# Kernel tuning notes

Measured on AMD Instinct MI355X. Metric: run time of the kernel, lower is better.

The kernel has to match this reference:

```python
import jax, jax.numpy as jnp
import numpy as np

N_NODES, N_EDGES = 1024, 4096
D_NODE, D_EDGE, HEADS, N_CLASSES = 128, 256, 4, 16


def setup_inputs() -> dict:
    key = jax.random.key(0)
    ks = jax.random.split(key, 32)
    def w(i, shape):
        return jax.random.normal(ks[i], shape, dtype=jnp.float32) * 0.02
    inp = {
        'node_features': jax.random.normal(ks[0], (N_NODES, D_NODE), dtype=jnp.float32),
        'edge_features': jax.random.normal(ks[1], (N_EDGES, D_EDGE), dtype=jnp.float32),
        'edge_index': jax.random.randint(ks[2], (2, N_EDGES), 0, N_NODES, dtype=jnp.int32),
    }
    i = 3
    for pre in ('a1', 'a2'):
        for nm, shape in [('Wn', (2 * D_NODE, D_EDGE)), ('Wq', (D_EDGE, D_EDGE)),
                          ('Wk', (D_EDGE, D_EDGE)), ('Wv', (D_EDGE, D_EDGE)), ('Wo', (D_EDGE, D_EDGE))]:
            inp[f'{pre}_{nm}'] = w(i, shape); i += 1
            inp[f'{pre}_b{nm[1:].lower()}'] = jnp.zeros((shape[1],), jnp.float32)
    inp['cls_W1'] = w(i, (D_EDGE, D_EDGE)); i += 1
    inp['cls_b1'] = jnp.zeros((D_EDGE,), jnp.float32)
    inp['cls_W2'] = w(i, (D_EDGE, N_CLASSES)); i += 1
    inp['cls_b2'] = jnp.zeros((N_CLASSES,), jnp.float32)
    return inp


def _edge_adjacency(edge_index):
    # edges adjacent iff they share an endpoint (hops=1). [E,E] bool
    src, dst = edge_index[0], edge_index[1]
    return ((src[:, None] == src[None, :]) | (src[:, None] == dst[None, :]) |
            (dst[:, None] == src[None, :]) | (dst[:, None] == dst[None, :]))


def _edge_attention(ef, nf, edge_index, adj, Wn, bn, Wq, bq, Wk, bk, Wv, bv, Wo, bo):
    src, dst = edge_index[0], edge_index[1]
    # gather endpoint node features and fuse into edge representation
    ctx = jnp.concatenate([nf[src], nf[dst]], axis=-1) @ Wn + bn  # [E, D_EDGE]
    x = ef + ctx
    E, D = x.shape
    hd = D // HEADS
    q = (x @ Wq + bq).reshape(E, HEADS, hd)
    k = (x @ Wk + bk).reshape(E, HEADS, hd)
    v = (x @ Wv + bv).reshape(E, HEADS, hd)
    scores = jnp.einsum('ehd,fhd->hef', q, k) / np.float32(np.sqrt(hd))  # [H,E,E]
    scores = jnp.where(adj[None, :, :], scores, jnp.float32(-1e9))
    attn = jax.nn.softmax(scores, axis=-1)
    out = jnp.einsum('hef,fhd->ehd', attn, v).reshape(E, D)
    return x + out @ Wo + bo


def reference(node_features, edge_features, edge_index,
              a1_Wn, a1_bn, a1_Wq, a1_bq, a1_Wk, a1_bk, a1_Wv, a1_bv, a1_Wo, a1_bo,
              a2_Wn, a2_bn, a2_Wq, a2_bq, a2_Wk, a2_bk, a2_Wv, a2_bv, a2_Wo, a2_bo,
              cls_W1, cls_b1, cls_W2, cls_b2):
    adj = _edge_adjacency(edge_index)
    ef = _edge_attention(edge_features, node_features, edge_index, adj,
                         a1_Wn, a1_bn, a1_Wq, a1_bq, a1_Wk, a1_bk, a1_Wv, a1_bv, a1_Wo, a1_bo)
    ef = _edge_attention(ef, node_features, edge_index, adj,
                         a2_Wn, a2_bn, a2_Wq, a2_bq, a2_Wk, a2_bk, a2_Wv, a2_bv, a2_Wo, a2_bo)
    h = jax.nn.gelu(ef @ cls_W1 + cls_b1, approximate=False)
    return h @ cls_W2 + cls_b2
```

## Files before the change

### kernel.cpp

```cpp
#include <hip/hip_runtime.h>
#include <math.h>

#define E_EDGES 4096
#define N_NODES 1024
#define D_NODE 128
#define D_EDGE 256
#define HEADS 4
#define HD 64
#define N_CLASSES 16
#define CAP 128

typedef __attribute__((ext_vector_type(8))) short short8v;
typedef __attribute__((ext_vector_type(4))) short short4v;
typedef __attribute__((ext_vector_type(4))) float f32x4;

__device__ __forceinline__ unsigned short f2bf(float f) {
    unsigned u = __float_as_uint(f);
    return (unsigned short)((u + 0x7FFFu + ((u >> 16) & 1u)) >> 16);
}
__device__ __forceinline__ float bf2f(unsigned short b) {
    return __uint_as_float(((unsigned)b) << 16);
}

__device__ __forceinline__ void gload_lds16(const void* g, void* l) {
    __builtin_amdgcn_global_load_lds((const __attribute__((address_space(1))) void*)g,
                                     (__attribute__((address_space(3))) void*)l, 16, 0, 0);
}

__device__ __forceinline__ void split_unit(
    char* smem, const float* __restrict__ W, short* __restrict__ ho,
    short* __restrict__ lo, int tile)
{
    float* tl = (float*)smem;
    const int t = threadIdx.x;
    const int k0 = (tile >> 2) * 64, n0 = (tile & 3) * 64;
#pragma unroll
    for (int p = 0; p < 4; ++p) {
        const int kr = (t >> 4) + p * 16;
        const int nc = (t & 15) * 4;
        *(float4*)&tl[kr * 65 + nc] = *(const float4*)&W[(size_t)(k0 + kr) * 256 + n0 + nc];
    }
    __syncthreads();
    const int n = t >> 2, ks = (t & 3) * 16;
    short8v h0, h1, l0, l1;
#pragma unroll
    for (int j = 0; j < 8; ++j) {
        const float x = tl[(ks + j) * 65 + n];
        const unsigned short hb = f2bf(x);
        h0[j] = (short)hb; l0[j] = (short)f2bf(x - bf2f(hb));
    }
#pragma unroll
    for (int j = 0; j < 8; ++j) {
        const float x = tl[(ks + 8 + j) * 65 + n];
        const unsigned short hb = f2bf(x);
        h1[j] = (short)hb; l1[j] = (short)f2bf(x - bf2f(hb));
    }
    *(short8v*)&ho[(size_t)(n0 + n) * 256 + k0 + ks] = h0;
    *(short8v*)&ho[(size_t)(n0 + n) * 256 + k0 + ks + 8] = h1;
    *(short8v*)&lo[(size_t)(n0 + n) * 256 + k0 + ks] = l0;
    *(short8v*)&lo[(size_t)(n0 + n) * 256 + k0 + ks + 8] = l1;
}

__device__ __forceinline__ void adj_unit(
    const int* __restrict__ src, const int* __restrict__ dst,
    int* __restrict__ cand, int* __restrict__ ccount, int e, int lane)
{
    const int a = src[e], b = dst[e];
    int* my = cand + (size_t)e * CAP;
    int base = 0;
    for (int c0 = 0; c0 < E_EDGES; c0 += 64) {
        const int f = c0 + lane;
        const int sf = src[f], df = dst[f];
        const bool adj = (sf == a) | (sf == b) | (df == a) | (df == b);
        const unsigned long long mk = __ballot(adj);
        if (adj) {
            const int pos = base + __popcll(mk & ((1ull << lane) - 1ull));
            if (pos < CAP) my[pos] = f;
        }
        base += __popcll(mk);
    }
    if (lane == 0) ccount[e] = (base < CAP) ? base : CAP;
}

__device__ __forceinline__ void mcore32(
    char* smem,
    const float* __restrict__ A, const float* __restrict__ A2,
    const short* __restrict__ BhiT, const short* __restrict__ BloT,
    const float* __restrict__ bias, const float* __restrict__ res,
    const float* __restrict__ res2, float* __restrict__ C,
    int m0, int n0,
    const float* __restrict__ nf, const int* __restrict__ src,
    const int* __restrict__ dst, int act)
{
    short* AsH = (short*)smem;
    short* AsL = (short*)(smem + 5120);
    short* BsH = (short*)(smem + 10240);
    short* BsL = (short*)(smem + 18432);
    const int t = threadIdx.x;
    const int w = t >> 6, lane = t & 63, lr = lane & 15, lg = lane >> 4;
    const int WR = (w >> 1) * 16, WC = (w & 1) * 32;
    const int ar = t >> 3, akc = (t & 7) * 4;
    const int bn = t >> 2, bkc = (t & 3) * 8;

    int nS = 0, nD = 0;
    if (nf) { nS = src[m0 + ar]; nD = dst[m0 + ar]; }

    f32x4 acc0 = {0.f, 0.f, 0.f, 0.f}, acc1 = {0.f, 0.f, 0.f, 0.f};
    float4 av;

#define LOADA_R(k0)                                                            \
    do {                                                                       \
        const int kq = (k0) + akc;                                             \
        if (nf) {                                                              \
            const float* pp = (kq < D_NODE)                                    \
                ? &nf[(size_t)nS * D_NODE + kq]                                \
                : &nf[(size_t)nD * D_NODE + kq - D_NODE];                      \
            av = *(const float4*)pp;                                           \
        } else {                                                               \
            av = *(const float4*)&A[(size_t)(m0 + ar) * 256 + kq];             \
            if (A2) {                                                          \
                const float4 c_ = *(const float4*)&A2[(size_t)(m0 + ar) * 256 + kq]; \
                av.x += c_.x; av.y += c_.y; av.z += c_.z; av.w += c_.w;        \
            }                                                                  \
        }                                                                      \
    } while (0)
#define STOREA_S(buf)                                                          \
    do {                                                                       \
        short4v ah, al;                                                        \
        const float fv[4] = {av.x, av.y, av.z, av.w};                          \
        _Pragma("unroll") for (int j = 0; j < 4; ++j) {                        \
            const unsigned short hb = f2bf(fv[j]);                             \
            ah[j] = (short)hb; al[j] = (short)f2bf(fv[j] - bf2f(hb));          \
        }                                                                      \
        *(short4v*)&AsH[(buf) * 1280 + ar * 40 + akc] = ah;                    \
        *(short4v*)&AsL[(buf) * 1280 + ar * 40 + akc] = al;                    \
    } while (0)
#define STAGE_B(buf, k0)                                                       \
    do {                                                                       \
        gload_lds16(&BhiT[(size_t)(n0 + bn) * 256 + (k0) + bkc],               \
                    BsH + (buf) * 2048 + t * 8);                               \
        gload_lds16(&BloT[(size_t)(n0 + bn) * 256 + (k0) + bkc],               \
                    BsL + (buf) * 2048 + t * 8);                               \
    } while (0)
#define MFMA_STEP(buf)                                                         \
    do {                                                                       \
        const int c0 = WC + lr, c1 = WC + 16 + lr;                             \
        const short8v bH0 = *(const short8v*)&BsH[(buf) * 2048 + c0 * 32 + lg * 8]; \
        const short8v bL0 = *(const short8v*)&BsL[(buf) * 2048 + c0 * 32 + lg * 8]; \
        const short8v bH1 = *(const short8v*)&BsH[(buf) * 2048 + c1 * 32 + lg * 8]; \
        const short8v bL1 = *(const short8v*)&BsL[(buf) * 2048 + c1 * 32 + lg * 8]; \
        const short8v aH = *(const short8v*)&AsH[(buf) * 1280 + (WR + lr) * 40 + lg * 8]; \
        const short8v aL = *(const short8v*)&AsL[(buf) * 1280 + (WR + lr) * 40 + lg * 8]; \
        acc0 = __builtin_amdgcn_mfma_f32_16x16x32_bf16(aH, bH0, acc0, 0, 0, 0);\
        acc1 = __builtin_amdgcn_mfma_f32_16x16x32_bf16(aH, bH1, acc1, 0, 0, 0);\
        acc0 = __builtin_amdgcn_mfma_f32_16x16x32_bf16(aH, bL0, acc0, 0, 0, 0);\
        acc1 = __builtin_amdgcn_mfma_f32_16x16x32_bf16(aH, bL1, acc1, 0, 0, 0);\
        acc0 = __builtin_amdgcn_mfma_f32_16x16x32_bf16(aL, bH0, acc0, 0, 0, 0);\
        acc1 = __builtin_amdgcn_mfma_f32_16x16x32_bf16(aL, bH1, acc1, 0, 0, 0);\
    } while (0)

    LOADA_R(0);
    STAGE_B(0, 0);
    STOREA_S(0);
    __syncthreads();

    for (int kt = 0; kt < 8; ++kt) {
        const int cur = kt & 1;
        if (kt < 7) {
            STAGE_B(cur ^ 1, (kt + 1) * 32);
            LOADA_R((kt + 1) * 32);
        }
        MFMA_STEP(cur);
        if (kt < 7) STOREA_S(cur ^ 1);
        __syncthreads();
    }

#define EPI(accv, ct)                                                          \
    do {                                                                       \
        const int col = n0 + WC + (ct) * 16 + lr;                              \
        const float bb = bias ? bias[col] : 0.f;                               \
        _Pragma("unroll") for (int i = 0; i < 4; ++i) {                        \
            const int row = m0 + WR + lg * 4 + i;                              \
            float v = accv[i] + bb;                                            \
            if (res)  v += res[(size_t)row * D_EDGE + col];                    \
            if (res2) v += res2[(size_t)row * D_EDGE + col];                   \
            if (act == 1) v = 0.5f * v * (1.f + erff(v * 0.70710678118654752f)); \
            C[(size_t)row * D_EDGE + col] = v;                                 \
        }                                                                      \
    } while (0)
    EPI(acc0, 0); EPI(acc1, 1);
#undef LOADA_R
#undef STOREA_S
#undef STAGE_B
#undef MFMA_STEP
#undef EPI
}

__global__ __launch_bounds__(256) void adj_prep(
    const int* __restrict__ src, const int* __restrict__ dst,
    int* __restrict__ cand, int* __restrict__ ccount,
    const float* Wn1, const float* Wn2, short* hiT, short* loT)
{
    __shared__ __attribute__((aligned(16))) char smem[16640];
    if (blockIdx.x < 1024) {
        const int t = threadIdx.x;
        adj_unit(src, dst, cand, ccount, blockIdx.x * 4 + (t >> 6), t & 63);
    } else {
        const int u = blockIdx.x - 1024;
        const int mat = (u >> 4) ? 5 : 0;
        split_unit(smem, (u >> 4) ? Wn2 : Wn1,
                   hiT + (size_t)mat * 65536, loT + (size_t)mat * 65536, u & 15);
    }
}

__global__ __launch_bounds__(256) void ctx_prep(
    const float* __restrict__ nf, const int* __restrict__ src,
    const int* __restrict__ dst, short* hiT, short* loT,
    const float* __restrict__ bn1, const float* __restrict__ bn2,
    float* __restrict__ ctx,
    const float* Wq1, const float* Wk1, const float* Wv1, const float* Wo1,
    const float* Wq2, const float* Wk2, const float* Wv2, const float* Wo2,
    const float* Wc1)
{
    __shared__ __attribute__((aligned(16))) char smem[26624];
    if (blockIdx.x < 1024) {
        const int lid = blockIdx.x;
        const int g = lid & 7, s = lid >> 3;
        const int rowt = g * 32 + (s >> 2);
        const int ct = s & 3;
        const int R = rowt * 32;
        const int Lyr = R >> 12;
        const int r = R & (E_EDGES - 1);
        mcore32(smem, nullptr, nullptr,
                hiT + (size_t)(Lyr * 5) * 65536, loT + (size_t)(Lyr * 5) * 65536,
                Lyr ? bn2 : bn1, nullptr, nullptr,
                ctx + (size_t)Lyr * E_EDGES * D_EDGE,
                r, ct * 64, nf, src, dst, 0);
    } else {
        const int u = blockIdx.x - 1024;
        const int mi = u >> 4;
        const int matIdx[9] = {1, 2, 3, 4, 6, 7, 8, 9, 10};
        const float* Ws[9] = {Wq1, Wk1, Wv1, Wo1, Wq2, Wk2, Wv2, Wo2, Wc1};
        const int mat = matIdx[mi];
        split_unit(smem, Ws[mi], hiT + (size_t)mat * 65536,
                   loT + (size_t)mat * 65536, u & 15);
    }
}

__global__ __launch_bounds__(256) void gemm_qkv32(
    const float* __restrict__ ef_in, const float* __restrict__ ctx,
    const short* __restrict__ whiT, const short* __restrict__ wloT,
    const float* __restrict__ bq, const float* __restrict__ bk,
    const float* __restrict__ bv,
    float* __restrict__ qb, float* __restrict__ kb, float* __restrict__ vb,
    int wbase)
{
    __shared__ __attribute__((aligned(16))) char smem[26624];
    const int lid = blockIdx.x;
    const int g = lid & 7, s = lid >> 3;
    const int rowt = g * 16 + s / 12;
    const int rem = s % 12, wsel = rem >> 2, ct = rem & 3;
    const short* BH = whiT + (size_t)(wbase + 1 + wsel) * 65536;
    const short* BL = wloT + (size_t)(wbase + 1 + wsel) * 65536;
    const float* bias = (wsel == 0) ? bq : (wsel == 1) ? bk : bv;
    float* C = (wsel == 0) ? qb : (wsel == 1) ? kb : vb;
    mcore32(smem, ef_in, ctx, BH, BL, bias, nullptr, nullptr, C,
            rowt * 32, ct * 64, nullptr, nullptr, nullptr, 0);
}

__global__ __launch_bounds__(256) void gemm_g32(
    const float* __restrict__ A, const short* __restrict__ BhiT,
    const short* __restrict__ BloT, const float* __restrict__ bias,
    const float* __restrict__ res, const float* __restrict__ res2,
    float* __restrict__ C, int act)
{
    __shared__ __attribute__((aligned(16))) char smem[26624];
    const int lid = blockIdx.x;
    const int g = lid & 7, s = lid >> 3;
    const int rowt = g * 16 + (s >> 2);
    const int ct = s & 3;
    mcore32(smem, A, nullptr, BhiT, BloT, bias, res, res2, C,
            rowt * 32, ct * 64, nullptr, nullptr, nullptr, act);
}

__global__ __launch_bounds__(256) void attn_sparse4(
    const float* __restrict__ q, const float* __restrict__ k,
    const float* __restrict__ v, const int* __restrict__ cand,
    const int* __restrict__ ccount, float* __restrict__ out)
{
    __shared__ int lc[CAP];
    const int e = blockIdx.x;
    const int t = threadIdx.x, h = t >> 6, lane = t & 63;
    const int g = lane >> 4, il = lane & 15;
    const int m = ccount[e];
    if (t < m) lc[t] = cand[(size_t)e * CAP + t];
    __syncthreads();

    const float4 q4 = *(const float4*)&q[(size_t)e * D_EDGE + h * HD + il * 4];
    float M = -1e30f, L = 0.f;
    float4 O = make_float4(0.f, 0.f, 0.f, 0.f);

    for (int i0 = g; i0 < m; i0 += 8) {
        const int f0 = lc[i0];
        const bool ok1 = (i0 + 4) < m;
        const int f1 = ok1 ? lc[i0 + 4] : f0;
        const float4 k0 = *(const float4*)&k[(size_t)f0 * D_EDGE + h * HD + il * 4];
        const float4 v0 = *(const float4*)&v[(size_t)f0 * D_EDGE + h * HD + il * 4];
        const float4 k1 = *(const float4*)&k[(size_t)f1 * D_EDGE + h * HD + il * 4];
        const float4 v1 = *(const float4*)&v[(size_t)f1 * D_EDGE + h * HD + il * 4];
        float s0 = q4.x * k0.x + q4.y * k0.y + q4.z * k0.z + q4.w * k0.w;
        float s1 = q4.x * k1.x + q4.y * k1.y + q4.z * k1.z + q4.w * k1.w;
        s0 += __shfl_xor(s0, 1); s1 += __shfl_xor(s1, 1);
        s0 += __shfl_xor(s0, 2); s1 += __shfl_xor(s1, 2);
        s0 += __shfl_xor(s0, 4); s1 += __shfl_xor(s1, 4);
        s0 += __shfl_xor(s0, 8); s1 += __shfl_xor(s1, 8);
        s0 *= 0.125f;
        s1 = ok1 ? s1 * 0.125f : -1e30f;
        const float Mn = fmaxf(M, fmaxf(s0, s1));
        const float al = __expf(M - Mn);
        const float p0 = __expf(s0 - Mn), p1 = __expf(s1 - Mn);
        O.x = O.x * al + p0 * v0.x + p1 * v1.x;
        O.y = O.y * al + p0 * v0.y + p1 * v1.y;
        O.z = O.z * al + p0 * v0.z + p1 * v1.z;
        O.w = O.w * al + p0 * v0.w + p1 * v1.w;
        L = L * al + p0 + p1;
        M = Mn;
    }
    float Mo = fmaxf(M, __shfl_xor(M, 16));
    Mo = fmaxf(Mo, __shfl_xor(Mo, 32));
    const float sc = __expf(M - Mo);
    O.x *= sc; O.y *= sc; O.z *= sc; O.w *= sc; L *= sc;
    O.x += __shfl_xor(O.x, 16); O.y += __shfl_xor(O.y, 16);
    O.z += __shfl_xor(O.z, 16); O.w += __shfl_xor(O.w, 16);
    L += __shfl_xor(L, 16);
    O.x += __shfl_xor(O.x, 32); O.y += __shfl_xor(O.y, 32);
    O.z += __shfl_xor(O.z, 32); O.w += __shfl_xor(O.w, 32);
    L += __shfl_xor(L, 32);
    if (lane < 16) {
        const float invL = 1.f / L;
        float4 r = make_float4(O.x * invL, O.y * invL, O.z * invL, O.w * invL);
        *(float4*)&out[(size_t)e * D_EDGE + h * HD + il * 4] = r;
    }
}

__global__ __launch_bounds__(256) void cls_out(
    const float* __restrict__ h, const float* __restrict__ W2,
    const float* __restrict__ b2, float* __restrict__ outp)
{
    __shared__ __attribute__((aligned(16))) float W2s[256 * 16];
    const int t = threadIdx.x;
    const int w = t >> 6, lane = t & 63, lr = lane & 15, lg = lane >> 4;
    const int m0 = blockIdx.x * 16;
#pragma unroll
    for (int p = 0; p < 4; ++p) {
        const int idx = t + 256 * p;
        gload_lds16(&W2[(size_t)idx * 4], W2s + (size_t)idx * 4);
    }
    __syncthreads();
    if (w == 0) {
        f32x4 o = {0.f, 0.f, 0.f, 0.f};
#pragma unroll
        for (int kk = 0; kk < 8; ++kk) {
            const float4 h0 = *(const float4*)&h[(size_t)(m0 + lr) * 256 + kk * 32 + lg * 8];
            const float4 h1 = *(const float4*)&h[(size_t)(m0 + lr) * 256 + kk * 32 + lg * 8 + 4];
            short8v aH, aL;
            const float fv[8] = {h0.x, h0.y, h0.z, h0.w, h1.x, h1.y, h1.z, h1.w};
#pragma unroll
            for (int j = 0; j < 8; ++j) {
                const unsigned short hb = f2bf(fv[j]);
                aH[j] = (short)hb; aL[j] = (short)f2bf(fv[j] - bf2f(hb));
            }
            short8v bH, bL;
#pragma unroll
            for (int j = 0; j < 8; ++j) {
                const float x = W2s[(size_t)(kk * 32 + lg * 8 + j) * 16 + lr];
                const unsigned short hb = f2bf(x);
                bH[j] = (short)hb; bL[j] = (short)f2bf(x - bf2f(hb));
            }
            o = __builtin_amdgcn_mfma_f32_16x16x32_bf16(aH, bH, o, 0, 0, 0);
            o = __builtin_amdgcn_mfma_f32_16x16x32_bf16(aH, bL, o, 0, 0, 0);
            o = __builtin_amdgcn_mfma_f32_16x16x32_bf16(aL, bH, o, 0, 0, 0);
        }
#pragma unroll
        for (int i = 0; i < 4; ++i) {
            const int row = m0 + lg * 4 + i;
            outp[(size_t)row * 16 + lr] = o[i] + b2[lr];
        }
    }
}

extern "C" void kernel_launch(void* const* d_in, const int* in_sizes, int n_in,
                              void* d_out, int out_size, void* d_ws, size_t ws_size,
                              hipStream_t stream)
{
    const float* nf = (const float*)d_in[0];
    const float* ef = (const float*)d_in[1];
    const int* ei = (const int*)d_in[2];
    const int* src = ei;
    const int* dst = ei + E_EDGES;

    const float* a_Wn[2] = {(const float*)d_in[3],  (const float*)d_in[13]};
    const float* a_bn[2] = {(const float*)d_in[4],  (const float*)d_in[14]};
    const float* a_Wq[2] = {(const float*)d_in[5],  (const float*)d_in[15]};
    const float* a_bq[2] = {(const float*)d_in[6],  (const float*)d_in[16]};
    const float* a_Wk[2] = {(const float*)d_in[7],  (const float*)d_in[17]};
    const float* a_bk[2] = {(const float*)d_in[8],  (const float*)d_in[18]};
    const float* a_Wv[2] = {(const float*)d_in[9],  (const float*)d_in[19]};
    const float* a_bv[2] = {(const float*)d_in[10], (const float*)d_in[20]};
    const float* a_Wo[2] = {(const float*)d_in[11], (const float*)d_in[21]};
    const float* a_bo[2] = {(const float*)d_in[12], (const float*)d_in[22]};
    const float* cls_W1 = (const float*)d_in[23];
    const float* cls_b1 = (const float*)d_in[24];
    const float* cls_W2 = (const float*)d_in[25];
    const float* cls_b2 = (const float*)d_in[26];

    const size_t buf = (size_t)E_EDGES * D_EDGE;
    float* ws = (float*)d_ws;
    float* ctx1 = ws + 0 * buf;
    float* ctx2 = ws + 1 * buf;
    float* qb   = ws + 2 * buf;
    float* kb   = ws + 3 * buf;
    float* vb   = ws + 4 * buf;
    float* ao   = ws + 5 * buf;
    float* y1   = ws + 6 * buf;
    float* y2   = ctx1;
    float* hb   = qb;
    int* cand   = (int*)(ws + 7 * buf);
    int* ccount = cand + (size_t)E_EDGES * CAP;
    short* whiT = (short*)(ccount + E_EDGES);
    short* wloT = whiT + (size_t)11 * 65536;

    adj_prep<<<1056, 256, 0, stream>>>(src, dst, cand, ccount,
                                       a_Wn[0], a_Wn[1], whiT, wloT);
    ctx_prep<<<1168, 256, 0, stream>>>(nf, src, dst, whiT, wloT,
                                       a_bn[0], a_bn[1], ctx1,
                                       a_Wq[0], a_Wk[0], a_Wv[0], a_Wo[0],
                                       a_Wq[1], a_Wk[1], a_Wv[1], a_Wo[1],
                                       cls_W1);

    const float* ef_in = ef;
    const float* ctxL[2] = {ctx1, ctx2};
    float* yout[2] = {y1, y2};
    for (int L = 0; L < 2; ++L) {
        const int wbase = L * 5;
        gemm_qkv32<<<1536, 256, 0, stream>>>(
            ef_in, ctxL[L], whiT, wloT, a_bq[L], a_bk[L], a_bv[L],
            qb, kb, vb, wbase);
        attn_sparse4<<<E_EDGES, 256, 0, stream>>>(qb, kb, vb, cand, ccount, ao);
        gemm_g32<<<512, 256, 0, stream>>>(
            ao, whiT + (size_t)(wbase + 4) * 65536,
            wloT + (size_t)(wbase + 4) * 65536,
            a_bo[L], ef_in, ctxL[L], yout[L], 0);
        ef_in = yout[L];
    }

    gemm_g32<<<512, 256, 0, stream>>>(
        y2, whiT + (size_t)10 * 65536, wloT + (size_t)10 * 65536,
        cls_b1, nullptr, nullptr, hb, 1);
    cls_out<<<E_EDGES / 16, 256, 0, stream>>>(hb, cls_W2, cls_b2, (float*)d_out);
}
```

Measured before the change: 129.0 us.

## Switch GEMM core to 32x32x16 MFMA with 128-thread blocks; regroup prep kernels

The shared GEMM core now uses 2 waves, each computing a 32x32 tile with the 32x32x16 bf16 MFMA instead of 4 waves of 16x16x32 MFMAs. Each thread loads and splits 8 A values, and issues two B staging loads per buffer. The aim is fewer MFMA issues and fewer LDS fragment reads per output. The prep stage is reorganised so that adjacency building and all weight hi/lo splits run in one kernel, followed by a separate context GEMM kernel. The trade-off is fewer threads per block, which means less latency hiding, and the context GEMM loses the overlap it previously had with weight splitting.

```diff
diff --git a/kernel.cpp b/kernel.cpp
--- a/kernel.cpp
+++ b/kernel.cpp
@@ -11,8 +11,8 @@
 #define CAP 128
 
 typedef __attribute__((ext_vector_type(8))) short short8v;
-typedef __attribute__((ext_vector_type(4))) short short4v;
 typedef __attribute__((ext_vector_type(4))) float f32x4;
+typedef __attribute__((ext_vector_type(16))) float f32x16;
 
 __device__ __forceinline__ unsigned short f2bf(float f) {
     unsigned u = __float_as_uint(f);
@@ -82,7 +82,28 @@
     if (lane == 0) ccount[e] = (base < CAP) ? base : CAP;
 }
 
-__device__ __forceinline__ void mcore32(
+__global__ __launch_bounds__(256) void prep(
+    const int* __restrict__ src, const int* __restrict__ dst,
+    int* __restrict__ cand, int* __restrict__ ccount,
+    const float* W0, const float* W1, const float* W2, const float* W3,
+    const float* W4, const float* W5, const float* W6, const float* W7,
+    const float* W8, const float* W9, const float* W10,
+    short* hiT, short* loT)
+{
+    __shared__ __attribute__((aligned(16))) char smem[16640];
+    if (blockIdx.x < 1024) {
+        const int t = threadIdx.x;
+        adj_unit(src, dst, cand, ccount, blockIdx.x * 4 + (t >> 6), t & 63);
+    } else {
+        const float* Ws[11] = {W0, W1, W2, W3, W4, W5, W6, W7, W8, W9, W10};
+        const int u = blockIdx.x - 1024;
+        const int mat = u >> 4;
+        split_unit(smem, Ws[mat], hiT + (size_t)mat * 65536,
+                   loT + (size_t)mat * 65536, u & 15);
+    }
+}
+
+__device__ __forceinline__ void mcore32b(
     char* smem,
     const float* __restrict__ A, const float* __restrict__ A2,
     const short* __restrict__ BhiT, const short* __restrict__ BloT,
@@ -97,16 +118,17 @@
     short* BsH = (short*)(smem + 10240);
     short* BsL = (short*)(smem + 18432);
     const int t = threadIdx.x;
-    const int w = t >> 6, lane = t & 63, lr = lane & 15, lg = lane >> 4;
-    const int WR = (w >> 1) * 16, WC = (w & 1) * 32;
-    const int ar = t >> 3, akc = (t & 7) * 4;
-    const int bn = t >> 2, bkc = (t & 3) * 8;
+    const int w = t >> 6, lane = t & 63;
+    const int lc = lane & 31, kb = lane >> 5;
+    const int WC = w * 32;
+    const int ar = t >> 2, akc = (t & 3) * 8;
 
     int nS = 0, nD = 0;
     if (nf) { nS = src[m0 + ar]; nD = dst[m0 + ar]; }
 
-    f32x4 acc0 = {0.f, 0.f, 0.f, 0.f}, acc1 = {0.f, 0.f, 0.f, 0.f};
-    float4 av;
+    f32x16 acc = {0.f, 0.f, 0.f, 0.f, 0.f, 0.f, 0.f, 0.f,
+                  0.f, 0.f, 0.f, 0.f, 0.f, 0.f, 0.f, 0.f};
+    float4 av0, av1;
 
 #define LOADA_R(k0)                                                            \
     do {                                                                       \
@@ -115,49 +137,50 @@
             const float* pp = (kq < D_NODE)                                    \
                 ? &nf[(size_t)nS * D_NODE + kq]                                \
                 : &nf[(size_t)nD * D_NODE + kq - D_NODE];                      \
-            av = *(const float4*)pp;                                           \
+            av0 = *(const float4*)pp; av1 = *(const float4*)(pp + 4);          \
         } else {                                                               \
-            av = *(const float4*)&A[(size_t)(m0 + ar) * 256 + kq];             \
+            av0 = *(const float4*)&A[(size_t)(m0 + ar) * 256 + kq];            \
+            av1 = *(const float4*)&A[(size_t)(m0 + ar) * 256 + kq + 4];        \
             if (A2) {                                                          \
-                const float4 c_ = *(const float4*)&A2[(size_t)(m0 + ar) * 256 + kq]; \
-                av.x += c_.x; av.y += c_.y; av.z += c_.z; av.w += c_.w;        \
+                const float4 c0_ = *(const float4*)&A2[(size_t)(m0 + ar) * 256 + kq];     \
+                const float4 c1_ = *(const float4*)&A2[(size_t)(m0 + ar) * 256 + kq + 4]; \
+                av0.x += c0_.x; av0.y += c0_.y; av0.z += c0_.z; av0.w += c0_.w; \
+                av1.x += c1_.x; av1.y += c1_.y; av1.z += c1_.z; av1.w += c1_.w; \
             }                                                                  \
         }                                                                      \
     } while (0)
 #define STOREA_S(buf)                                                          \
     do {                                                                       \
-        short4v ah, al;                                                        \
-        const float fv[4] = {av.x, av.y, av.z, av.w};                          \
-        _Pragma("unroll") for (int j = 0; j < 4; ++j) {                        \
+        short8v ah, al;                                                        \
+        const float fv[8] = {av0.x, av0.y, av0.z, av0.w,                       \
+                             av1.x, av1.y, av1.z, av1.w};                      \
+        _Pragma("unroll") for (int j = 0; j < 8; ++j) {                        \
             const unsigned short hb = f2bf(fv[j]);                             \
             ah[j] = (short)hb; al[j] = (short)f2bf(fv[j] - bf2f(hb));          \
         }                                                                      \
-        *(short4v*)&AsH[(buf) * 1280 + ar * 40 + akc] = ah;                    \
-        *(short4v*)&AsL[(buf) * 1280 + ar * 40 + akc] = al;                    \
+        *(short8v*)&AsH[(buf) * 1280 + ar * 40 + akc] = ah;                    \
+        *(short8v*)&AsL[(buf) * 1280 + ar * 40 + akc] = al;                    \
     } while (0)
 #define STAGE_B(buf, k0)                                                       \
-    do {                                                                       \
-        gload_lds16(&BhiT[(size_t)(n0 + bn) * 256 + (k0) + bkc],               \
-                    BsH + (buf) * 2048 + t * 8);                               \
-        gload_lds16(&BloT[(size_t)(n0 + bn) * 256 + (k0) + bkc],               \
-                    BsL + (buf) * 2048 + t * 8);                               \
-    } while (0)
+    do { _Pragma("unroll") for (int p = 0; p < 2; ++p) {                       \
+        const int idx = t + 128 * p;                                           \
+        const int cc = idx >> 2, k8 = (idx & 3) * 8;                           \
+        gload_lds16(&BhiT[(size_t)(n0 + cc) * 256 + (k0) + k8],                \
+                    BsH + (buf) * 2048 + (size_t)idx * 8);                     \
+        gload_lds16(&BloT[(size_t)(n0 + cc) * 256 + (k0) + k8],                \
+                    BsL + (buf) * 2048 + (size_t)idx * 8);                     \
+    } } while (0)
 #define MFMA_STEP(buf)                                                         \
-    do {                                                                       \
-        const int c0 = WC + lr, c1 = WC + 16 + lr;                             \
-        const short8v bH0 = *(const short8v*)&BsH[(buf) * 2048 + c0 * 32 + lg * 8]; \
-        const short8v bL0 = *(const short8v*)&BsL[(buf) * 2048 + c0 * 32 + lg * 8]; \
-        const short8v bH1 = *(const short8v*)&BsH[(buf) * 2048 + c1 * 32 + lg * 8]; \
-        const short8v bL1 = *(const short8v*)&BsL[(buf) * 2048 + c1 * 32 + lg * 8]; \
-        const short8v aH = *(const short8v*)&AsH[(buf) * 1280 + (WR + lr) * 40 + lg * 8]; \
-        const short8v aL = *(const short8v*)&AsL[(buf) * 1280 + (WR + lr) * 40 + lg * 8]; \
-        acc0 = __builtin_amdgcn_mfma_f32_16x16x32_bf16(aH, bH0, acc0, 0, 0, 0);\
-        acc1 = __builtin_amdgcn_mfma_f32_16x16x32_bf16(aH, bH1, acc1, 0, 0, 0);\
-        acc0 = __builtin_amdgcn_mfma_f32_16x16x32_bf16(aH, bL0, acc0, 0, 0, 0);\
-        acc1 = __builtin_amdgcn_mfma_f32_16x16x32_bf16(aH, bL1, acc1, 0, 0, 0);\
-        acc0 = __builtin_amdgcn_mfma_f32_16x16x32_bf16(aL, bH0, acc0, 0, 0, 0);\
-        acc1 = __builtin_amdgcn_mfma_f32_16x16x32_bf16(aL, bH1, acc1, 0, 0, 0);\
-    } while (0)
+    do { _Pragma("unroll") for (int s = 0; s < 2; ++s) {                       \
+        const int ko = s * 16 + kb * 8;                                        \
+        const short8v aH = *(const short8v*)&AsH[(buf) * 1280 + lc * 40 + ko]; \
+        const short8v aL = *(const short8v*)&AsL[(buf) * 1280 + lc * 40 + ko]; \
+        const short8v bH = *(const short8v*)&BsH[(buf) * 2048 + (WC + lc) * 32 + ko]; \
+        const short8v bL = *(const short8v*)&BsL[(buf) * 2048 + (WC + lc) * 32 + ko]; \
+        acc = __builtin_amdgcn_mfma_f32_32x32x16_bf16(aH, bH, acc, 0, 0, 0);   \
+        acc = __builtin_amdgcn_mfma_f32_32x32x16_bf16(aH, bL, acc, 0, 0, 0);   \
+        acc = __builtin_amdgcn_mfma_f32_32x32x16_bf16(aL, bH, acc, 0, 0, 0);   \
+    } } while (0)
 
     LOADA_R(0);
     STAGE_B(0, 0);
@@ -175,79 +198,47 @@
         __syncthreads();
     }
 
-#define EPI(accv, ct)                                                          \
-    do {                                                                       \
-        const int col = n0 + WC + (ct) * 16 + lr;                              \
-        const float bb = bias ? bias[col] : 0.f;                               \
-        _Pragma("unroll") for (int i = 0; i < 4; ++i) {                        \
-            const int row = m0 + WR + lg * 4 + i;                              \
-            float v = accv[i] + bb;                                            \
-            if (res)  v += res[(size_t)row * D_EDGE + col];                    \
-            if (res2) v += res2[(size_t)row * D_EDGE + col];                   \
-            if (act == 1) v = 0.5f * v * (1.f + erff(v * 0.70710678118654752f)); \
-            C[(size_t)row * D_EDGE + col] = v;                                 \
-        }                                                                      \
-    } while (0)
-    EPI(acc0, 0); EPI(acc1, 1);
+    {
+        const int col = n0 + WC + lc;
+        const float bb = bias ? bias[col] : 0.f;
+#pragma unroll
+        for (int r = 0; r < 16; ++r) {
+            const int row = m0 + (r & 3) + 8 * (r >> 2) + 4 * kb;
+            float v = acc[r] + bb;
+            if (res)  v += res[(size_t)row * D_EDGE + col];
+            if (res2) v += res2[(size_t)row * D_EDGE + col];
+            if (act == 1) v = 0.5f * v * (1.f + erff(v * 0.70710678118654752f));
+            C[(size_t)row * D_EDGE + col] = v;
+        }
+    }
 #undef LOADA_R
 #undef STOREA_S
 #undef STAGE_B
 #undef MFMA_STEP
-#undef EPI
-}
-
-__global__ __launch_bounds__(256) void adj_prep(
-    const int* __restrict__ src, const int* __restrict__ dst,
-    int* __restrict__ cand, int* __restrict__ ccount,
-    const float* Wn1, const float* Wn2, short* hiT, short* loT)
-{
-    __shared__ __attribute__((aligned(16))) char smem[16640];
-    if (blockIdx.x < 1024) {
-        const int t = threadIdx.x;
-        adj_unit(src, dst, cand, ccount, blockIdx.x * 4 + (t >> 6), t & 63);
-    } else {
-        const int u = blockIdx.x - 1024;
-        const int mat = (u >> 4) ? 5 : 0;
-        split_unit(smem, (u >> 4) ? Wn2 : Wn1,
-                   hiT + (size_t)mat * 65536, loT + (size_t)mat * 65536, u & 15);
-    }
-}
-
-__global__ __launch_bounds__(256) void ctx_prep(
+}
+
+__global__ __launch_bounds__(128) void gemm_ctx32(
     const float* __restrict__ nf, const int* __restrict__ src,
-    const int* __restrict__ dst, short* hiT, short* loT,
-    const float* __restrict__ bn1, const float* __restrict__ bn2,
-    float* __restrict__ ctx,
-    const float* Wq1, const float* Wk1, const float* Wv1, const float* Wo1,
-    const float* Wq2, const float* Wk2, const float* Wv2, const float* Wo2,
-    const float* Wc1)
+    const int* __restrict__ dst, const short* __restrict__ whiT,
+    const short* __restrict__ wloT, const float* __restrict__ bn1,
+    const float* __restrict__ bn2, float* __restrict__ ctx)
 {
     __shared__ __attribute__((aligned(16))) char smem[26624];
-    if (blockIdx.x < 1024) {
-        const int lid = blockIdx.x;
-        const int g = lid & 7, s = lid >> 3;
-        const int rowt = g * 32 + (s >> 2);
-        const int ct = s & 3;
-        const int R = rowt * 32;
-        const int Lyr = R >> 12;
-        const int r = R & (E_EDGES - 1);
-        mcore32(smem, nullptr, nullptr,
-                hiT + (size_t)(Lyr * 5) * 65536, loT + (size_t)(Lyr * 5) * 65536,
-                Lyr ? bn2 : bn1, nullptr, nullptr,
-                ctx + (size_t)Lyr * E_EDGES * D_EDGE,
-                r, ct * 64, nf, src, dst, 0);
-    } else {
-        const int u = blockIdx.x - 1024;
-        const int mi = u >> 4;
-        const int matIdx[9] = {1, 2, 3, 4, 6, 7, 8, 9, 10};
-        const float* Ws[9] = {Wq1, Wk1, Wv1, Wo1, Wq2, Wk2, Wv2, Wo2, Wc1};
-        const int mat = matIdx[mi];
-        split_unit(smem, Ws[mi], hiT + (size_t)mat * 65536,
-                   loT + (size_t)mat * 65536, u & 15);
-    }
-}
-
-__global__ __launch_bounds__(256) void gemm_qkv32(
+    const int lid = blockIdx.x;
+    const int g = lid & 7, s = lid >> 3;
+    const int rowt = g * 32 + (s >> 2);
+    const int ct = s & 3;
+    const int R = rowt * 32;
+    const int Lyr = R >> 12;
+    const int r = R & (E_EDGES - 1);
+    mcore32b(smem, nullptr, nullptr,
+             whiT + (size_t)(Lyr * 5) * 65536, wloT + (size_t)(Lyr * 5) * 65536,
+             Lyr ? bn2 : bn1, nullptr, nullptr,
+             ctx + (size_t)Lyr * E_EDGES * D_EDGE,
+             r, ct * 64, nf, src, dst, 0);
+}
+
+__global__ __launch_bounds__(128) void gemm_qkv32(
     const float* __restrict__ ef_in, const float* __restrict__ ctx,
     const short* __restrict__ whiT, const short* __restrict__ wloT,
     const float* __restrict__ bq, const float* __restrict__ bk,
@@ -264,11 +255,11 @@
     const short* BL = wloT + (size_t)(wbase + 1 + wsel) * 65536;
     const float* bias = (wsel == 0) ? bq : (wsel == 1) ? bk : bv;
     float* C = (wsel == 0) ? qb : (wsel == 1) ? kb : vb;
-    mcore32(smem, ef_in, ctx, BH, BL, bias, nullptr, nullptr, C,
-            rowt * 32, ct * 64, nullptr, nullptr, nullptr, 0);
-}
-
-__global__ __launch_bounds__(256) void gemm_g32(
+    mcore32b(smem, ef_in, ctx, BH, BL, bias, nullptr, nullptr, C,
+             rowt * 32, ct * 64, nullptr, nullptr, nullptr, 0);
+}
+
+__global__ __launch_bounds__(128) void gemm_g32(
     const float* __restrict__ A, const short* __restrict__ BhiT,
     const short* __restrict__ BloT, const float* __restrict__ bias,
     const float* __restrict__ res, const float* __restrict__ res2,
@@ -279,8 +270,8 @@
     const int g = lid & 7, s = lid >> 3;
     const int rowt = g * 16 + (s >> 2);
     const int ct = s & 3;
-    mcore32(smem, A, nullptr, BhiT, BloT, bias, res, res2, C,
-            rowt * 32, ct * 64, nullptr, nullptr, nullptr, act);
+    mcore32b(smem, A, nullptr, BhiT, BloT, bias, res, res2, C,
+             rowt * 32, ct * 64, nullptr, nullptr, nullptr, act);
 }
 
 __global__ __launch_bounds__(256) void attn_sparse4(
@@ -430,31 +421,30 @@
     short* whiT = (short*)(ccount + E_EDGES);
     short* wloT = whiT + (size_t)11 * 65536;
 
-    adj_prep<<<1056, 256, 0, stream>>>(src, dst, cand, ccount,
-                                       a_Wn[0], a_Wn[1], whiT, wloT);
-    ctx_prep<<<1168, 256, 0, stream>>>(nf, src, dst, whiT, wloT,
-                                       a_bn[0], a_bn[1], ctx1,
-                                       a_Wq[0], a_Wk[0], a_Wv[0], a_Wo[0],
-                                       a_Wq[1], a_Wk[1], a_Wv[1], a_Wo[1],
-                                       cls_W1);
+    prep<<<1200, 256, 0, stream>>>(src, dst, cand, ccount,
+                                   a_Wn[0], a_Wq[0], a_Wk[0], a_Wv[0], a_Wo[0],
+                                   a_Wn[1], a_Wq[1], a_Wk[1], a_Wv[1], a_Wo[1],
+                                   cls_W1, whiT, wloT);
+    gemm_ctx32<<<1024, 128, 0, stream>>>(nf, src, dst, whiT, wloT,
+                                         a_bn[0], a_bn[1], ctx1);
 
     const float* ef_in = ef;
     const float* ctxL[2] = {ctx1, ctx2};
     float* yout[2] = {y1, y2};
     for (int L = 0; L < 2; ++L) {
         const int wbase = L * 5;
-        gemm_qkv32<<<1536, 256, 0, stream>>>(
+        gemm_qkv32<<<1536, 128, 0, stream>>>(
             ef_in, ctxL[L], whiT, wloT, a_bq[L], a_bk[L], a_bv[L],
             qb, kb, vb, wbase);
         attn_sparse4<<<E_EDGES, 256, 0, stream>>>(qb, kb, vb, cand, ccount, ao);
-        gemm_g32<<<512, 256, 0, stream>>>(
+        gemm_g32<<<512, 128, 0, stream>>>(
             ao, whiT + (size_t)(wbase + 4) * 65536,
             wloT + (size_t)(wbase + 4) * 65536,
             a_bo[L], ef_in, ctxL[L], yout[L], 0);
         ef_in = yout[L];
     }
 
-    gemm_g32<<<512, 256, 0, stream>>>(
+    gemm_g32<<<512, 128, 0, stream>>>(
         y2, whiT + (size_t)10 * 65536, wloT + (size_t)10 * 65536,
         cls_b1, nullptr, nullptr, hb, 1);
     cls_out<<<E_EDGES / 16, 256, 0, stream>>>(hb, cls_W2, cls_b2, (float*)d_out);
```

After: 141.0 us. +9.3%, slower.

## Map one wavefront per edge covering all heads in sparse attention

Applied to the files above, without the earlier changes.

The sparse edge attention kernel now gives each 64-lane wavefront one edge, with 16 lanes per head and four edges per block, instead of one 256-thread block per edge that split candidates across lane groups. Each wave walks the whole candidate list two at a time, with a scalar tail, so the cross-group max/sum merge shuffles and the block barrier go away. Each iteration also loads the full 1KB K/V row contiguously. The cost is a longer serial loop per edge and less latency hiding within one edge's work.

```diff
diff --git a/kernel.cpp b/kernel.cpp
--- a/kernel.cpp
+++ b/kernel.cpp
@@ -283,27 +283,26 @@
             rowt * 32, ct * 64, nullptr, nullptr, nullptr, act);
 }
 
-__global__ __launch_bounds__(256) void attn_sparse4(
+__global__ __launch_bounds__(256) void attn_sparse5(
     const float* __restrict__ q, const float* __restrict__ k,
     const float* __restrict__ v, const int* __restrict__ cand,
     const int* __restrict__ ccount, float* __restrict__ out)
 {
-    __shared__ int lc[CAP];
-    const int e = blockIdx.x;
-    const int t = threadIdx.x, h = t >> 6, lane = t & 63;
-    const int g = lane >> 4, il = lane & 15;
+    __shared__ int lc[4][CAP];
+    const int t = threadIdx.x;
+    const int w = t >> 6, lane = t & 63;
+    const int e = blockIdx.x * 4 + w;
+    const int h = lane >> 4, il = lane & 15;
     const int m = ccount[e];
-    if (t < m) lc[t] = cand[(size_t)e * CAP + t];
-    __syncthreads();
+    for (int i = lane; i < m; i += 64) lc[w][i] = cand[(size_t)e * CAP + i];
 
     const float4 q4 = *(const float4*)&q[(size_t)e * D_EDGE + h * HD + il * 4];
     float M = -1e30f, L = 0.f;
     float4 O = make_float4(0.f, 0.f, 0.f, 0.f);
 
-    for (int i0 = g; i0 < m; i0 += 8) {
-        const int f0 = lc[i0];
-        const bool ok1 = (i0 + 4) < m;
-        const int f1 = ok1 ? lc[i0 + 4] : f0;
+    int i = 0;
+    for (; i + 2 <= m; i += 2) {
+        const int f0 = lc[w][i], f1 = lc[w][i + 1];
         const float4 k0 = *(const float4*)&k[(size_t)f0 * D_EDGE + h * HD + il * 4];
         const float4 v0 = *(const float4*)&v[(size_t)f0 * D_EDGE + h * HD + il * 4];
         const float4 k1 = *(const float4*)&k[(size_t)f1 * D_EDGE + h * HD + il * 4];
@@ -314,8 +313,7 @@
         s0 += __shfl_xor(s0, 2); s1 += __shfl_xor(s1, 2);
         s0 += __shfl_xor(s0, 4); s1 += __shfl_xor(s1, 4);
         s0 += __shfl_xor(s0, 8); s1 += __shfl_xor(s1, 8);
-        s0 *= 0.125f;
-        s1 = ok1 ? s1 * 0.125f : -1e30f;
+        s0 *= 0.125f; s1 *= 0.125f;
         const float Mn = fmaxf(M, fmaxf(s0, s1));
         const float al = __expf(M - Mn);
         const float p0 = __expf(s0 - Mn), p1 = __expf(s1 - Mn);
@@ -326,21 +324,29 @@
         L = L * al + p0 + p1;
         M = Mn;
     }
-    float Mo = fmaxf(M, __shfl_xor(M, 16));
-    Mo = fmaxf(Mo, __shfl_xor(Mo, 32));
-    const float sc = __expf(M - Mo);
-    O.x *= sc; O.y *= sc; O.z *= sc; O.w *= sc; L *= sc;
-    O.x += __shfl_xor(O.x, 16); O.y += __shfl_xor(O.y, 16);
-    O.z += __shfl_xor(O.z, 16); O.w += __shfl_xor(O.w, 16);
-    L += __shfl_xor(L, 16);
-    O.x += __shfl_xor(O.x, 32); O.y += __shfl_xor(O.y, 32);
-    O.z += __shfl_xor(O.z, 32); O.w += __shfl_xor(O.w, 32);
-    L += __shfl_xor(L, 32);
-    if (lane < 16) {
-        const float invL = 1.f / L;
-        float4 r = make_float4(O.x * invL, O.y * invL, O.z * invL, O.w * invL);
-        *(float4*)&out[(size_t)e * D_EDGE + h * HD + il * 4] = r;
-    }
+    if (i < m) {
+        const int f = lc[w][i];
+        const float4 kv = *(const float4*)&k[(size_t)f * D_EDGE + h * HD + il * 4];
+        const float4 vv = *(const float4*)&v[(size_t)f * D_EDGE + h * HD + il * 4];
+        float s = q4.x * kv.x + q4.y * kv.y + q4.z * kv.z + q4.w * kv.w;
+        s += __shfl_xor(s, 1);
+        s += __shfl_xor(s, 2);
+        s += __shfl_xor(s, 4);
+        s += __shfl_xor(s, 8);
+        s *= 0.125f;
+        const float Mn = fmaxf(M, s);
+        const float al = __expf(M - Mn);
+        const float p = __expf(s - Mn);
+        O.x = O.x * al + p * vv.x;
+        O.y = O.y * al + p * vv.y;
+        O.z = O.z * al + p * vv.z;
+        O.w = O.w * al + p * vv.w;
+        L = L * al + p;
+        M = Mn;
+    }
+    const float invL = 1.f / L;
+    float4 r = make_float4(O.x * invL, O.y * invL, O.z * invL, O.w * invL);
+    *(float4*)&out[(size_t)e * D_EDGE + h * HD + il * 4] = r;
 }
 
 __global__ __launch_bounds__(256) void cls_out(
@@ -446,7 +452,7 @@
         gemm_qkv32<<<1536, 256, 0, stream>>>(
             ef_in, ctxL[L], whiT, wloT, a_bq[L], a_bk[L], a_bv[L],
             qb, kb, vb, wbase);
-        attn_sparse4<<<E_EDGES, 256, 0, stream>>>(qb, kb, vb, cand, ccount, ao);
+        attn_sparse5<<<E_EDGES / 4, 256, 0, stream>>>(qb, kb, vb, cand, ccount, ao);
         gemm_g32<<<512, 256, 0, stream>>>(
             ao, whiT + (size_t)(wbase + 4) * 65536,
             wloT + (size_t)(wbase + 4) * 65536,
```

New measurement: 123.3 us, median of 2. 1.05x faster.
